# Performance work log

Measured on AMD Instinct MI355X. Metric: run time of the kernel, lower is better.

Reference implementation:

```python
import jax, jax.numpy as jnp
import numpy as np

B = 64            # number of graphs
N = 2048          # nodes per graph (equal segments; torch.stack in the original requires this)
D = 256           # hidden_dim
G = 4             # num_groups
SUBS = 3          # subclasses per group -> num_classes = 12
C = G * SUBS


def _layer_norm(x, g, b, eps=1e-5):
    mu = jnp.mean(x, axis=-1, keepdims=True)
    var = jnp.var(x, axis=-1, keepdims=True)
    return (x - mu) * jax.lax.rsqrt(var + eps) * g + b


def setup_inputs() -> dict:
    key = jax.random.key(0)
    ks = jax.random.split(key, 20)
    T = B * N
    inp = {
        "node_features": jax.random.normal(ks[0], (T, D), dtype=jnp.float32),
        "batch": jnp.repeat(jnp.arange(B, dtype=jnp.int64), N),  # sorted, equal-size segments
        # group queries (nn.Parameter randn)
        "group_queries": jax.random.normal(ks[1], (G, D), dtype=jnp.float32),
        # per-group projector MLP: D -> 2D -> SUBS*D (stacked over groups)
        "proj_w1": jax.random.normal(ks[2], (G, D, 2 * D), dtype=jnp.float32) * (1.0 / np.sqrt(D)),
        "proj_b1": jnp.zeros((G, 2 * D), dtype=jnp.float32),
        "proj_w2": jax.random.normal(ks[3], (G, 2 * D, SUBS * D), dtype=jnp.float32) * (1.0 / np.sqrt(2 * D)),
        "proj_b2": jnp.zeros((G, SUBS * D), dtype=jnp.float32),
        # output_proj_12: LN -> Linear(D, D//2) -> ReLU -> Linear(D//2, 1)
        "ln12_g": jnp.ones((D,), dtype=jnp.float32),
        "ln12_b": jnp.zeros((D,), dtype=jnp.float32),
        "w12a": jax.random.normal(ks[4], (D, D // 2), dtype=jnp.float32) * (1.0 / np.sqrt(D)),
        "b12a": jnp.zeros((D // 2,), dtype=jnp.float32),
        "w12b": jax.random.normal(ks[5], (D // 2, 1), dtype=jnp.float32) * (1.0 / np.sqrt(D // 2)),
        "b12b": jnp.zeros((1,), dtype=jnp.float32),
        # output_proj_4
        "ln4_g": jnp.ones((D,), dtype=jnp.float32),
        "ln4_b": jnp.zeros((D,), dtype=jnp.float32),
        "w4a": jax.random.normal(ks[6], (D, D // 2), dtype=jnp.float32) * (1.0 / np.sqrt(D)),
        "b4a": jnp.zeros((D // 2,), dtype=jnp.float32),
        "w4b": jax.random.normal(ks[7], (D // 2, 1), dtype=jnp.float32) * (1.0 / np.sqrt(D // 2)),
        "b4b": jnp.zeros((1,), dtype=jnp.float32),
    }
    return inp


def reference(node_features, batch, group_queries, proj_w1, proj_b1, proj_w2, proj_b2,
              ln12_g, ln12_b, w12a, b12a, w12b, b12b,
              ln4_g, ln4_b, w4a, b4a, w4b, b4b):
    # --- derive class queries from group queries (per-group MLP) ---
    h = jax.nn.relu(jnp.einsum('gd,gdh->gh', group_queries, proj_w1) + proj_b1)   # [G, 2D]
    flat = jnp.einsum('gh,ghk->gk', h, proj_w2) + proj_b2                         # [G, SUBS*D]
    # group g maps to global class indices [3g, 3g+1, 3g+2] -> simple reshape gives ordered queries
    class_queries = flat.reshape(C, D)                                            # [12, D]

    scale = jnp.asarray(D ** 0.5, node_features.dtype)
    # equal-size sorted segments: reshape total nodes into [B, N, D] per-graph blocks
    nodes = node_features.reshape(B, N, D)

    # --- 12-class attention pooling ---
    scores12 = jnp.einsum('cd,bnd->bcn', class_queries, nodes) / scale            # [B, 12, N]
    attn12 = jax.nn.softmax(scores12, axis=-1)
    pooled12 = jnp.einsum('bcn,bnd->bcd', attn12, nodes)                          # [B, 12, D]
    x12 = _layer_norm(pooled12, ln12_g, ln12_b)
    logits_12 = (jax.nn.relu(x12 @ w12a + b12a) @ w12b + b12b)[..., 0]            # [B, 12]

    # --- 4-group attention pooling ---
    scores4 = jnp.einsum('gd,bnd->bgn', group_queries, nodes) / scale             # [B, 4, N]
    attn4 = jax.nn.softmax(scores4, axis=-1)
    pooled4 = jnp.einsum('bgn,bnd->bgd', attn4, nodes)                            # [B, 4, D]
    x4 = _layer_norm(pooled4, ln4_g, ln4_b)
    logits_4 = (jax.nn.relu(x4 @ w4a + b4a) @ w4b + b4b)[..., 0]                  # [B, 4]

    return (logits_12, logits_4, attn12)
```

## Files before the change

### kernel.cpp

```cpp
#include <hip/hip_runtime.h>
#include <math.h>

#define BG   64
#define NN   2048
#define DD   256
#define CQ   16
#define PP   16

static constexpr size_t WS_Q16 = 0;
static constexpr size_t WS_H   = 4096;
static constexpr size_t WS_S   = 6144;
static constexpr size_t WS_P   = 6144 + (size_t)BG * CQ * NN;

__global__ __launch_bounds__(256) void kA1(const float* __restrict__ gq,
                                           const float* __restrict__ w1,
                                           const float* __restrict__ b1,
                                           float* __restrict__ ws) {
    int blk = blockIdx.x;
    int g   = blk >> 4;
    int jb  = (blk & 15) * 32;
    int t   = threadIdx.x;
    __shared__ float qlds[256];
    qlds[t] = gq[g * 256 + t];
    if ((blk & 15) == 0) ws[WS_Q16 + (12 + g) * 256 + t] = gq[g * 256 + t];
    __syncthreads();
    int jl = t & 31, dp = t >> 5;
    float acc = 0.f;
    const float* wp = w1 + ((size_t)g * 256) * 512 + jb + jl;
    for (int i = 0; i < 32; ++i) {
        int d = dp * 32 + i;
        acc += qlds[d] * wp[(size_t)d * 512];
    }
    __shared__ float red[8][33];
    red[dp][jl] = acc;
    __syncthreads();
    if (dp == 0) {
        float s = 0.f;
        for (int p = 0; p < 8; ++p) s += red[p][jl];
        s += b1[g * 512 + jb + jl];
        ws[WS_H + g * 512 + jb + jl] = fmaxf(s, 0.f);
    }
}

__global__ __launch_bounds__(256) void kA2(const float* __restrict__ w2,
                                           const float* __restrict__ b2,
                                           float* __restrict__ ws) {
    int blk = blockIdx.x;
    int g   = blk / 48;
    int kb  = (blk % 48) * 16;
    int t   = threadIdx.x;
    __shared__ float hlds[512];
    hlds[t]       = ws[WS_H + g * 512 + t];
    hlds[t + 256] = ws[WS_H + g * 512 + t + 256];
    __syncthreads();
    int kl = t & 15, dp = t >> 4;
    float acc = 0.f;
    const float* wp = w2 + ((size_t)g * 512) * 768 + kb + kl;
    for (int i = 0; i < 32; ++i) {
        int jj = dp * 32 + i;
        acc += hlds[jj] * wp[(size_t)jj * 768];
    }
    __shared__ float red[16][17];
    red[dp][kl] = acc;
    __syncthreads();
    if (dp == 0) {
        float s = 0.f;
        for (int p = 0; p < 16; ++p) s += red[p][kl];
        ws[WS_Q16 + g * 768 + kb + kl] = s + b2[g * 768 + kb + kl];
    }
}

__global__ __launch_bounds__(256) void kB(const float* __restrict__ x,
                                          const float* __restrict__ q16,
                                          float* __restrict__ scores) {
    __shared__ float4 qlds[CQ * 64];
    int t = threadIdx.x;
    const float4* qg = (const float4*)q16;
    for (int i = 0; i < 4; ++i) qlds[t + i * 256] = qg[t + i * 256];
    __syncthreads();

    int n0 = blockIdx.x * 256;
    const float4* xa = (const float4*)x + (size_t)(n0 + t) * 64;

    float acc[CQ];
    #pragma unroll
    for (int c = 0; c < CQ; ++c) acc[c] = 0.f;

    float4 buf[8];
    #pragma unroll
    for (int i = 0; i < 8; ++i) buf[i] = xa[i];

    for (int base = 0; base < 64; base += 8) {
        float4 cur[8];
        #pragma unroll
        for (int i = 0; i < 8; ++i) cur[i] = buf[i];
        if (base + 8 < 64) {
            #pragma unroll
            for (int i = 0; i < 8; ++i) buf[i] = xa[base + 8 + i];
        }
        #pragma unroll
        for (int i = 0; i < 8; ++i) {
            #pragma unroll
            for (int c = 0; c < CQ; ++c) {
                float4 q = qlds[c * 64 + base + i];
                acc[c] += q.x * cur[i].x + q.y * cur[i].y
                        + q.z * cur[i].z + q.w * cur[i].w;
            }
        }
    }
    int bgi = n0 >> 11;
    int nl  = n0 & 2047;
    float* srow = scores + (size_t)bgi * CQ * NN + nl;
    #pragma unroll
    for (int c = 0; c < CQ; ++c) srow[(size_t)c * NN + t] = acc[c] * 0.0625f;
}

__global__ __launch_bounds__(256) void kC(float* __restrict__ scores,
                                          float* __restrict__ out_attn) {
    int bc = blockIdx.x;
    int b  = bc >> 4, c = bc & 15;
    int t  = threadIdx.x;
    int wave = t >> 6, lane = t & 63;
    float4* row = (float4*)(scores + (size_t)(b * CQ + c) * NN);
    float4 v1 = row[t];
    float4 v2 = row[t + 256];

    float m = fmaxf(fmaxf(fmaxf(v1.x, v1.y), fmaxf(v1.z, v1.w)),
                    fmaxf(fmaxf(v2.x, v2.y), fmaxf(v2.z, v2.w)));
    #pragma unroll
    for (int off = 32; off; off >>= 1) m = fmaxf(m, __shfl_xor(m, off, 64));
    __shared__ float wmax[4], wsum[4];
    if (lane == 0) wmax[wave] = m;
    __syncthreads();
    m = fmaxf(fmaxf(wmax[0], wmax[1]), fmaxf(wmax[2], wmax[3]));

    float4 e1, e2;
    e1.x = __expf(v1.x - m); e1.y = __expf(v1.y - m);
    e1.z = __expf(v1.z - m); e1.w = __expf(v1.w - m);
    e2.x = __expf(v2.x - m); e2.y = __expf(v2.y - m);
    e2.z = __expf(v2.z - m); e2.w = __expf(v2.w - m);
    float s = e1.x + e1.y + e1.z + e1.w + e2.x + e2.y + e2.z + e2.w;
    #pragma unroll
    for (int off = 32; off; off >>= 1) s += __shfl_xor(s, off, 64);
    if (lane == 0) wsum[wave] = s;
    __syncthreads();
    float inv = 1.f / (wsum[0] + wsum[1] + wsum[2] + wsum[3]);
    e1.x *= inv; e1.y *= inv; e1.z *= inv; e1.w *= inv;
    e2.x *= inv; e2.y *= inv; e2.z *= inv; e2.w *= inv;
    row[t]       = e1;
    row[t + 256] = e2;
    if (c < 12) {
        float4* ar = (float4*)out_attn + (size_t)(b * 12 + c) * (NN / 4);
        ar[t]       = e1;
        ar[t + 256] = e2;
    }
}

__global__ __launch_bounds__(256) void kD(const float* __restrict__ x,
                                          const float* __restrict__ p,
                                          float* __restrict__ partial) {
    constexpr int NPB = NN / PP;
    constexpr int NPW = NPB / 4;
    int blk = blockIdx.x;
    int b = blk / PP, part = blk % PP;
    int t = threadIdx.x, wave = t >> 6, lane = t & 63;

    float4 acc[CQ];
    #pragma unroll
    for (int c = 0; c < CQ; ++c) acc[c] = make_float4(0.f, 0.f, 0.f, 0.f);

    const float4* xf = (const float4*)x;
    const float4* pf = (const float4*)p;
    int nbase = part * NPB + wave * NPW;
    size_t xrow = ((size_t)b * NN + nbase) * 64 + lane;
    size_t prow = (size_t)b * CQ * (NN / 4) + (nbase >> 2);

    for (int nn = 0; nn < NPW; nn += 4) {
        float4 x0 = xf[xrow + (size_t)nn * 64];
        float4 x1 = xf[xrow + (size_t)(nn + 1) * 64];
        float4 x2 = xf[xrow + (size_t)(nn + 2) * 64];
        float4 x3 = xf[xrow + (size_t)(nn + 3) * 64];
        #pragma unroll
        for (int c = 0; c < CQ; ++c) {
            float4 pv = pf[prow + (size_t)c * (NN / 4) + (nn >> 2)];
            acc[c].x += pv.x * x0.x + pv.y * x1.x + pv.z * x2.x + pv.w * x3.x;
            acc[c].y += pv.x * x0.y + pv.y * x1.y + pv.z * x2.y + pv.w * x3.y;
            acc[c].z += pv.x * x0.z + pv.y * x1.z + pv.z * x2.z + pv.w * x3.z;
            acc[c].w += pv.x * x0.w + pv.y * x1.w + pv.z * x2.w + pv.w * x3.w;
        }
    }

    __shared__ float sdata[CQ * 256];
    for (int w = 0; w < 4; ++w) {
        if (wave == w) {
            #pragma unroll
            for (int c = 0; c < CQ; ++c) {
                float* dst = &sdata[c * 256 + lane * 4];
                if (w == 0) {
                    dst[0] = acc[c].x; dst[1] = acc[c].y;
                    dst[2] = acc[c].z; dst[3] = acc[c].w;
                } else {
                    dst[0] += acc[c].x; dst[1] += acc[c].y;
                    dst[2] += acc[c].z; dst[3] += acc[c].w;
                }
            }
        }
        __syncthreads();
    }
    float* po = partial + (size_t)blk * (CQ * 256);
    for (int i = t; i < CQ * 256; i += 256) po[i] = sdata[i];
}

__global__ __launch_bounds__(256) void kE(const float* __restrict__ partial,
        const float* __restrict__ lnG12, const float* __restrict__ lnB12,
        const float* __restrict__ wA12,  const float* __restrict__ bA12,
        const float* __restrict__ wB12,  const float* __restrict__ bB12,
        const float* __restrict__ lnG4,  const float* __restrict__ lnB4,
        const float* __restrict__ wA4,   const float* __restrict__ bA4,
        const float* __restrict__ wB4,   const float* __restrict__ bB4,
        float* __restrict__ out) {
    int bc = blockIdx.x;
    int b = bc >> 4, c = bc & 15;
    int t = threadIdx.x, wave = t >> 6, lane = t & 63;

    float v = 0.f;
    size_t base = ((size_t)b * PP * CQ + c) * 256 + t;
    for (int part = 0; part < PP; ++part) v += partial[base + (size_t)part * (CQ * 256)];

    __shared__ float wr1[4], wr2[4];
    float s = v;
    #pragma unroll
    for (int off = 32; off; off >>= 1) s += __shfl_xor(s, off, 64);
    if (lane == 0) wr1[wave] = s;
    __syncthreads();
    float mu = (wr1[0] + wr1[1] + wr1[2] + wr1[3]) * (1.f / 256.f);
    float dv = v - mu;
    s = dv * dv;
    #pragma unroll
    for (int off = 32; off; off >>= 1) s += __shfl_xor(s, off, 64);
    if (lane == 0) wr2[wave] = s;
    __syncthreads();
    float var = (wr2[0] + wr2[1] + wr2[2] + wr2[3]) * (1.f / 256.f);

    bool is12 = (c < 12);
    const float* lg = is12 ? lnG12 : lnG4;
    const float* lb = is12 ? lnB12 : lnB4;
    const float* wA = is12 ? wA12  : wA4;
    const float* bA = is12 ? bA12  : bA4;
    const float* wB = is12 ? wB12  : wB4;
    const float* bB = is12 ? bB12  : bB4;

    __shared__ float ylds[256];
    __shared__ float hred[256];
    __shared__ float hlds[128];
    float y = dv * rsqrtf(var + 1e-5f) * lg[t] + lb[t];
    ylds[t] = y;
    __syncthreads();
    {
        int j = t & 127, half = t >> 7;
        float hh = 0.f;
        const float* wc = wA + (size_t)half * 128 * 128 + j;
        for (int d = 0; d < 128; ++d) hh += ylds[half * 128 + d] * wc[(size_t)d * 128];
        hred[t] = hh;
    }
    __syncthreads();
    if (t < 128) hlds[t] = fmaxf(hred[t] + hred[t + 128] + bA[t], 0.f);
    __syncthreads();
    if (t < 64) {
        float pp = hlds[t] * wB[t] + hlds[t + 64] * wB[t + 64];
        #pragma unroll
        for (int off = 32; off; off >>= 1) pp += __shfl_xor(pp, off, 64);
        if (t == 0) {
            float logit = pp + bB[0];
            if (is12) out[b * 12 + c] = logit;
            else      out[768 + b * 4 + (c - 12)] = logit;
        }
    }
}

extern "C" void kernel_launch(void* const* d_in, const int* in_sizes, int n_in,
                              void* d_out, int out_size, void* d_ws, size_t ws_size,
                              hipStream_t stream) {
    const float* x     = (const float*)d_in[0];
    const float* gq    = (const float*)d_in[2];
    const float* w1    = (const float*)d_in[3];
    const float* b1    = (const float*)d_in[4];
    const float* w2    = (const float*)d_in[5];
    const float* b2    = (const float*)d_in[6];
    const float* ln12g = (const float*)d_in[7];
    const float* ln12b = (const float*)d_in[8];
    const float* w12a  = (const float*)d_in[9];
    const float* b12a  = (const float*)d_in[10];
    const float* w12b  = (const float*)d_in[11];
    const float* b12b  = (const float*)d_in[12];
    const float* ln4g  = (const float*)d_in[13];
    const float* ln4b  = (const float*)d_in[14];
    const float* w4a   = (const float*)d_in[15];
    const float* b4a   = (const float*)d_in[16];
    const float* w4b   = (const float*)d_in[17];
    const float* b4b   = (const float*)d_in[18];

    float* out     = (float*)d_out;
    float* ws      = (float*)d_ws;
    float* q16     = ws + WS_Q16;
    float* scores  = ws + WS_S;
    float* partial = ws + WS_P;

    kA1<<<64,  256, 0, stream>>>(gq, w1, b1, ws);
    kA2<<<192, 256, 0, stream>>>(w2, b2, ws);
    kB <<<512, 256, 0, stream>>>(x, q16, scores);
    kC <<<1024,256, 0, stream>>>(scores, out + 1024);
    kD <<<BG * PP, 256, 0, stream>>>(x, scores, partial);
    kE <<<1024, 256, 0, stream>>>(partial,
            ln12g, ln12b, w12a, b12a, w12b, b12b,
            ln4g,  ln4b,  w4a,  b4a,  w4b,  b4b, out);
}
```

Before: 305.7 us.

## Fuse scores, chunked online softmax and pooling into one flash-style kernel

Merges the score, softmax and weighted-pooling kernels into a single kernel per 256-node chunk. Each chunk computes local max and exp-sum and accumulates unnormalized pooled vectors. A final kernel rescales the chunk partials with the log-sum-exp merge, and a separate kernel writes the normalized attention output. This is meant to avoid re-reading node features and the score matrix across separate launches. In exchange it uses fewer blocks (512) for the pooling work and adds a serial merge step in kE. Some loop unroll pragmas are also added.

New measurement: 289.8 us. -5.2%, faster.

```diff
diff --git a/kernel.cpp b/kernel.cpp
--- a/kernel.cpp
+++ b/kernel.cpp
@@ -5,12 +5,15 @@
 #define NN   2048
 #define DD   256
 #define CQ   16
-#define PP   16
+#define NCH  8
 
 static constexpr size_t WS_Q16 = 0;
 static constexpr size_t WS_H   = 4096;
 static constexpr size_t WS_S   = 6144;
-static constexpr size_t WS_P   = 6144 + (size_t)BG * CQ * NN;
+static constexpr size_t WS_ML  = WS_S + (size_t)BG * CQ * NN;
+static constexpr size_t WS_PL  = WS_ML + (size_t)BG * NCH * 32;
+static constexpr size_t WS_FML = WS_PL + (size_t)BG * NCH * CQ * DD;
+static constexpr size_t WS_FIL = WS_FML + 1024;
 
 __global__ __launch_bounds__(256) void kA1(const float* __restrict__ gq,
                                            const float* __restrict__ w1,
@@ -27,6 +30,7 @@
     int jl = t & 31, dp = t >> 5;
     float acc = 0.f;
     const float* wp = w1 + ((size_t)g * 256) * 512 + jb + jl;
+    #pragma unroll 8
     for (int i = 0; i < 32; ++i) {
         int d = dp * 32 + i;
         acc += qlds[d] * wp[(size_t)d * 512];
@@ -36,6 +40,7 @@
     __syncthreads();
     if (dp == 0) {
         float s = 0.f;
+        #pragma unroll
         for (int p = 0; p < 8; ++p) s += red[p][jl];
         s += b1[g * 512 + jb + jl];
         ws[WS_H + g * 512 + jb + jl] = fmaxf(s, 0.f);
@@ -56,6 +61,7 @@
     int kl = t & 15, dp = t >> 4;
     float acc = 0.f;
     const float* wp = w2 + ((size_t)g * 512) * 768 + kb + kl;
+    #pragma unroll 8
     for (int i = 0; i < 32; ++i) {
         int jj = dp * 32 + i;
         acc += hlds[jj] * wp[(size_t)jj * 768];
@@ -65,31 +71,36 @@
     __syncthreads();
     if (dp == 0) {
         float s = 0.f;
+        #pragma unroll
         for (int p = 0; p < 16; ++p) s += red[p][kl];
         ws[WS_Q16 + g * 768 + kb + kl] = s + b2[g * 768 + kb + kl];
     }
 }
 
-__global__ __launch_bounds__(256) void kB(const float* __restrict__ x,
-                                          const float* __restrict__ q16,
-                                          float* __restrict__ scores) {
+__global__ __launch_bounds__(256) void kF(const float* __restrict__ x,
+                                          float* __restrict__ ws) {
     __shared__ float4 qlds[CQ * 64];
-    int t = threadIdx.x;
-    const float4* qg = (const float4*)q16;
+    __shared__ float  wlds[CQ * 256];
+    __shared__ float  mbuf[CQ], lbuf[CQ];
+
+    int t   = threadIdx.x;
+    int blk = blockIdx.x;
+    int b   = blk >> 3, ch = blk & 7;
+    int gn0 = b * NN + ch * 256;
+
+    const float4* qg = (const float4*)(ws + WS_Q16);
+    #pragma unroll
     for (int i = 0; i < 4; ++i) qlds[t + i * 256] = qg[t + i * 256];
     __syncthreads();
 
-    int n0 = blockIdx.x * 256;
-    const float4* xa = (const float4*)x + (size_t)(n0 + t) * 64;
-
-    float acc[CQ];
-    #pragma unroll
-    for (int c = 0; c < CQ; ++c) acc[c] = 0.f;
+    const float4* xa = (const float4*)x + (size_t)(gn0 + t) * 64;
+    float sc[CQ];
+    #pragma unroll
+    for (int c = 0; c < CQ; ++c) sc[c] = 0.f;
 
     float4 buf[8];
     #pragma unroll
     for (int i = 0; i < 8; ++i) buf[i] = xa[i];
-
     for (int base = 0; base < 64; base += 8) {
         float4 cur[8];
         #pragma unroll
@@ -103,94 +114,72 @@
             #pragma unroll
             for (int c = 0; c < CQ; ++c) {
                 float4 q = qlds[c * 64 + base + i];
-                acc[c] += q.x * cur[i].x + q.y * cur[i].y
-                        + q.z * cur[i].z + q.w * cur[i].w;
+                sc[c] += q.x * cur[i].x + q.y * cur[i].y
+                       + q.z * cur[i].z + q.w * cur[i].w;
             }
         }
     }
-    int bgi = n0 >> 11;
-    int nl  = n0 & 2047;
-    float* srow = scores + (size_t)bgi * CQ * NN + nl;
-    #pragma unroll
-    for (int c = 0; c < CQ; ++c) srow[(size_t)c * NN + t] = acc[c] * 0.0625f;
-}
-
-__global__ __launch_bounds__(256) void kC(float* __restrict__ scores,
-                                          float* __restrict__ out_attn) {
-    int bc = blockIdx.x;
-    int b  = bc >> 4, c = bc & 15;
-    int t  = threadIdx.x;
+    #pragma unroll
+    for (int c = 0; c < CQ; ++c) sc[c] *= 0.0625f;
+
+    float* srow = ws + WS_S + ((size_t)b * CQ) * NN + ch * 256;
+    #pragma unroll
+    for (int c = 0; c < CQ; ++c) srow[(size_t)c * NN + t] = sc[c];
+
+    #pragma unroll
+    for (int c = 0; c < CQ; ++c) wlds[c * 256 + t] = sc[c];
+    __syncthreads();
+    {
+        int c = t >> 4, slot = t & 15;
+        float mv = -1e30f;
+        #pragma unroll
+        for (int k = 0; k < 16; ++k) mv = fmaxf(mv, wlds[c * 256 + slot + k * 16]);
+        #pragma unroll
+        for (int off = 1; off < 16; off <<= 1) mv = fmaxf(mv, __shfl_xor(mv, off, 64));
+        if (slot == 0) mbuf[c] = mv;
+    }
+    __syncthreads();
+    #pragma unroll
+    for (int c = 0; c < CQ; ++c) wlds[c * 256 + t] = __expf(sc[c] - mbuf[c]);
+    __syncthreads();
+    {
+        int c = t >> 4, slot = t & 15;
+        float lv = 0.f;
+        #pragma unroll
+        for (int k = 0; k < 16; ++k) lv += wlds[c * 256 + slot + k * 16];
+        #pragma unroll
+        for (int off = 1; off < 16; off <<= 1) lv += __shfl_xor(lv, off, 64);
+        if (slot == 0) lbuf[c] = lv;
+    }
+    __syncthreads();
+    if (t < CQ) {
+        ws[WS_ML + (size_t)blk * 32 + t]      = mbuf[t];
+        ws[WS_ML + (size_t)blk * 32 + 16 + t] = lbuf[t];
+    }
+
     int wave = t >> 6, lane = t & 63;
-    float4* row = (float4*)(scores + (size_t)(b * CQ + c) * NN);
-    float4 v1 = row[t];
-    float4 v2 = row[t + 256];
-
-    float m = fmaxf(fmaxf(fmaxf(v1.x, v1.y), fmaxf(v1.z, v1.w)),
-                    fmaxf(fmaxf(v2.x, v2.y), fmaxf(v2.z, v2.w)));
-    #pragma unroll
-    for (int off = 32; off; off >>= 1) m = fmaxf(m, __shfl_xor(m, off, 64));
-    __shared__ float wmax[4], wsum[4];
-    if (lane == 0) wmax[wave] = m;
-    __syncthreads();
-    m = fmaxf(fmaxf(wmax[0], wmax[1]), fmaxf(wmax[2], wmax[3]));
-
-    float4 e1, e2;
-    e1.x = __expf(v1.x - m); e1.y = __expf(v1.y - m);
-    e1.z = __expf(v1.z - m); e1.w = __expf(v1.w - m);
-    e2.x = __expf(v2.x - m); e2.y = __expf(v2.y - m);
-    e2.z = __expf(v2.z - m); e2.w = __expf(v2.w - m);
-    float s = e1.x + e1.y + e1.z + e1.w + e2.x + e2.y + e2.z + e2.w;
-    #pragma unroll
-    for (int off = 32; off; off >>= 1) s += __shfl_xor(s, off, 64);
-    if (lane == 0) wsum[wave] = s;
-    __syncthreads();
-    float inv = 1.f / (wsum[0] + wsum[1] + wsum[2] + wsum[3]);
-    e1.x *= inv; e1.y *= inv; e1.z *= inv; e1.w *= inv;
-    e2.x *= inv; e2.y *= inv; e2.z *= inv; e2.w *= inv;
-    row[t]       = e1;
-    row[t + 256] = e2;
-    if (c < 12) {
-        float4* ar = (float4*)out_attn + (size_t)(b * 12 + c) * (NN / 4);
-        ar[t]       = e1;
-        ar[t + 256] = e2;
-    }
-}
-
-__global__ __launch_bounds__(256) void kD(const float* __restrict__ x,
-                                          const float* __restrict__ p,
-                                          float* __restrict__ partial) {
-    constexpr int NPB = NN / PP;
-    constexpr int NPW = NPB / 4;
-    int blk = blockIdx.x;
-    int b = blk / PP, part = blk % PP;
-    int t = threadIdx.x, wave = t >> 6, lane = t & 63;
-
     float4 acc[CQ];
     #pragma unroll
     for (int c = 0; c < CQ; ++c) acc[c] = make_float4(0.f, 0.f, 0.f, 0.f);
 
-    const float4* xf = (const float4*)x;
-    const float4* pf = (const float4*)p;
-    int nbase = part * NPB + wave * NPW;
-    size_t xrow = ((size_t)b * NN + nbase) * 64 + lane;
-    size_t prow = (size_t)b * CQ * (NN / 4) + (nbase >> 2);
-
-    for (int nn = 0; nn < NPW; nn += 4) {
-        float4 x0 = xf[xrow + (size_t)nn * 64];
-        float4 x1 = xf[xrow + (size_t)(nn + 1) * 64];
-        float4 x2 = xf[xrow + (size_t)(nn + 2) * 64];
-        float4 x3 = xf[xrow + (size_t)(nn + 3) * 64];
+    const float4* xq = (const float4*)x + (size_t)(gn0 + wave * 64) * 64 + lane;
+    for (int nq = 0; nq < 16; ++nq) {
+        float4 x0 = xq[(size_t)(nq * 4 + 0) * 64];
+        float4 x1 = xq[(size_t)(nq * 4 + 1) * 64];
+        float4 x2 = xq[(size_t)(nq * 4 + 2) * 64];
+        float4 x3 = xq[(size_t)(nq * 4 + 3) * 64];
         #pragma unroll
         for (int c = 0; c < CQ; ++c) {
-            float4 pv = pf[prow + (size_t)c * (NN / 4) + (nn >> 2)];
-            acc[c].x += pv.x * x0.x + pv.y * x1.x + pv.z * x2.x + pv.w * x3.x;
-            acc[c].y += pv.x * x0.y + pv.y * x1.y + pv.z * x2.y + pv.w * x3.y;
-            acc[c].z += pv.x * x0.z + pv.y * x1.z + pv.z * x2.z + pv.w * x3.z;
-            acc[c].w += pv.x * x0.w + pv.y * x1.w + pv.z * x2.w + pv.w * x3.w;
-        }
-    }
-
-    __shared__ float sdata[CQ * 256];
+            float4 ev = *(const float4*)&wlds[c * 256 + wave * 64 + nq * 4];
+            acc[c].x += ev.x * x0.x + ev.y * x1.x + ev.z * x2.x + ev.w * x3.x;
+            acc[c].y += ev.x * x0.y + ev.y * x1.y + ev.z * x2.y + ev.w * x3.y;
+            acc[c].z += ev.x * x0.z + ev.y * x1.z + ev.z * x2.z + ev.w * x3.z;
+            acc[c].w += ev.x * x0.w + ev.y * x1.w + ev.z * x2.w + ev.w * x3.w;
+        }
+    }
+
+    float* sdata = (float*)qlds;
+    __syncthreads();
     for (int w = 0; w < 4; ++w) {
         if (wave == w) {
             #pragma unroll
@@ -207,11 +196,12 @@
         }
         __syncthreads();
     }
-    float* po = partial + (size_t)blk * (CQ * 256);
-    for (int i = t; i < CQ * 256; i += 256) po[i] = sdata[i];
-}
-
-__global__ __launch_bounds__(256) void kE(const float* __restrict__ partial,
+    float* po = ws + WS_PL + (size_t)blk * (CQ * 256);
+    #pragma unroll
+    for (int i = 0; i < CQ; ++i) po[t + i * 256] = sdata[t + i * 256];
+}
+
+__global__ __launch_bounds__(256) void kE(float* __restrict__ ws,
         const float* __restrict__ lnG12, const float* __restrict__ lnB12,
         const float* __restrict__ wA12,  const float* __restrict__ bA12,
         const float* __restrict__ wB12,  const float* __restrict__ bB12,
@@ -223,9 +213,33 @@
     int b = bc >> 4, c = bc & 15;
     int t = threadIdx.x, wave = t >> 6, lane = t & 63;
 
+    __shared__ float scl[NCH];
+    __shared__ float sinvl;
+    if (t == 0) {
+        float mi[NCH], li[NCH];
+        float m = -1e30f;
+        for (int i = 0; i < NCH; ++i) {
+            mi[i] = ws[WS_ML + (size_t)(b * NCH + i) * 32 + c];
+            li[i] = ws[WS_ML + (size_t)(b * NCH + i) * 32 + 16 + c];
+            m = fmaxf(m, mi[i]);
+        }
+        float l = 0.f;
+        for (int i = 0; i < NCH; ++i) {
+            float s = __expf(mi[i] - m);
+            scl[i] = s;
+            l += s * li[i];
+        }
+        float il = 1.f / l;
+        sinvl = il;
+        ws[WS_FML + bc] = m;
+        ws[WS_FIL + bc] = il;
+    }
+    __syncthreads();
+
     float v = 0.f;
-    size_t base = ((size_t)b * PP * CQ + c) * 256 + t;
-    for (int part = 0; part < PP; ++part) v += partial[base + (size_t)part * (CQ * 256)];
+    for (int i = 0; i < NCH; ++i)
+        v += scl[i] * ws[WS_PL + ((size_t)(b * NCH + i) * CQ + c) * 256 + t];
+    v *= sinvl;
 
     __shared__ float wr1[4], wr2[4];
     float s = v;
@@ -260,6 +274,7 @@
         int j = t & 127, half = t >> 7;
         float hh = 0.f;
         const float* wc = wA + (size_t)half * 128 * 128 + j;
+        #pragma unroll 4
         for (int d = 0; d < 128; ++d) hh += ylds[half * 128 + d] * wc[(size_t)d * 128];
         hred[t] = hh;
     }
@@ -275,6 +290,27 @@
             if (is12) out[b * 12 + c] = logit;
             else      out[768 + b * 4 + (c - 12)] = logit;
         }
+    }
+}
+
+__global__ __launch_bounds__(256) void kAttn(const float* __restrict__ ws,
+                                             float* __restrict__ out_attn) {
+    int blk = blockIdx.x;
+    int b = blk / 12, c = blk % 12;
+    int t = threadIdx.x;
+    float m  = ws[WS_FML + b * 16 + c];
+    float il = ws[WS_FIL + b * 16 + c];
+    const float4* sr = (const float4*)(ws + WS_S + ((size_t)b * CQ + c) * NN);
+    float4* ar = (float4*)out_attn + (size_t)(b * 12 + c) * (NN / 4);
+    #pragma unroll
+    for (int k = 0; k < 2; ++k) {
+        float4 v = sr[t + k * 256];
+        float4 e;
+        e.x = __expf(v.x - m) * il;
+        e.y = __expf(v.y - m) * il;
+        e.z = __expf(v.z - m) * il;
+        e.w = __expf(v.w - m) * il;
+        ar[t + k * 256] = e;
     }
 }
 
@@ -300,18 +336,14 @@
     const float* w4b   = (const float*)d_in[17];
     const float* b4b   = (const float*)d_in[18];
 
-    float* out     = (float*)d_out;
-    float* ws      = (float*)d_ws;
-    float* q16     = ws + WS_Q16;
-    float* scores  = ws + WS_S;
-    float* partial = ws + WS_P;
-
-    kA1<<<64,  256, 0, stream>>>(gq, w1, b1, ws);
-    kA2<<<192, 256, 0, stream>>>(w2, b2, ws);
-    kB <<<512, 256, 0, stream>>>(x, q16, scores);
-    kC <<<1024,256, 0, stream>>>(scores, out + 1024);
-    kD <<<BG * PP, 256, 0, stream>>>(x, scores, partial);
-    kE <<<1024, 256, 0, stream>>>(partial,
+    float* out = (float*)d_out;
+    float* ws  = (float*)d_ws;
+
+    kA1  <<<64,       256, 0, stream>>>(gq, w1, b1, ws);
+    kA2  <<<192,      256, 0, stream>>>(w2, b2, ws);
+    kF   <<<BG * NCH, 256, 0, stream>>>(x, ws);
+    kE   <<<1024,     256, 0, stream>>>(ws,
             ln12g, ln12b, w12a, b12a, w12b, b12b,
             ln4g,  ln4b,  w4a,  b4a,  w4b,  b4b, out);
-}
+    kAttn<<<768,      256, 0, stream>>>(ws, out + 1024);
+}
```
